# Kernel tuning notes

Hardware: AMD Instinct MI355X
Metric: run time of the kernel (lower is better)

The kernel has to match this reference:

```python
import jax, jax.numpy as jnp
import numpy as np

B, C, H, W, HEADS = 4, 32, 384, 384, 8
EPS_LN = 1e-6


def conv2d(x, w, b=None, pad=0, groups=1):
    out = jax.lax.conv_general_dilated(
        x, w, window_strides=(1, 1), padding=[(pad, pad), (pad, pad)],
        dimension_numbers=('NCHW', 'OIHW', 'NCHW'), feature_group_count=groups)
    return out if b is None else out + b[None, :, None, None]


def setup_inputs() -> dict:
    key = jax.random.key(0)
    ks = jax.random.split(key, 24)
    p = lambda k, shape: jax.random.normal(k, shape, jnp.float32) * 0.05
    return {
        'x': jax.random.normal(ks[0], (B, C, H, W), jnp.float32),
        # MCC core params (bias=False)
        'ln_w': jnp.ones((C,), jnp.float32),
        'ln_b': jnp.zeros((C,), jnp.float32),
        'temperature': jnp.ones((HEADS, 1, 1), jnp.float32),
        'pw_w': p(ks[1], (3 * C, C, 1, 1)),
        'dw_w': p(ks[2], (3 * C, 1, 3, 3)),
        'proj_w': p(ks[3], (C, C, 1, 1)),
        'ff1_w': p(ks[4], (C, C, 1, 1)),
        'ffdw_w': p(ks[5], (C, 1, 3, 3)),
        # color-space detector (convs have default bias=True)
        'det_w1': p(ks[6], (64, 32, 3, 3)), 'det_b1': jnp.zeros((64,), jnp.float32),
        'det_w2': p(ks[7], (128, 64, 3, 3)), 'det_b2': jnp.zeros((128,), jnp.float32),
        'det_w3': p(ks[8], (256, 128, 3, 3)), 'det_b3': jnp.zeros((256,), jnp.float32),
        'det_fc_w': p(ks[9], (3, 256)), 'det_fc_b': jnp.zeros((3,), jnp.float32),
        # HVI->RGB model
        'hvi_w1': p(ks[10], (64, 32, 3, 3)), 'hvi_b1': jnp.zeros((64,), jnp.float32),
        'hvi_w2': p(ks[11], (32, 64, 3, 3)), 'hvi_b2': jnp.zeros((32,), jnp.float32),
        # YCbCr->RGB model
        'ycc_w1': p(ks[12], (64, 32, 3, 3)), 'ycc_b1': jnp.zeros((64,), jnp.float32),
        'ycc_w2': p(ks[13], (32, 64, 3, 3)), 'ycc_b2': jnp.zeros((32,), jnp.float32),
    }


def _mcc_forward(x, ln_w, ln_b, temperature, pw_w, dw_w, proj_w, ff1_w, ffdw_w,
                 det_w1, det_b1, det_w2, det_b2, det_w3, det_b3, det_fc_w, det_fc_b,
                 hvi_w1, hvi_b1, hvi_w2, hvi_b2, ycc_w1, ycc_b1, ycc_w2, ycc_b2):
    relu = jax.nn.relu
    # ---- auto color-space detection ----
    f = relu(conv2d(x, det_w1, det_b1, pad=1))
    f = relu(conv2d(f, det_w2, det_b2, pad=1))
    f = relu(conv2d(f, det_w3, det_b3, pad=1))
    f = f.mean(axis=(2, 3))                      # adaptive avg pool -> [B, 256]
    logits = f @ det_fc_w.T + det_fc_b           # [B, 3]
    pred = jnp.argmax(logits[0])                 # torch uses predicted[0].item()

    def rgb_branch(xx):
        return xx

    def hvi_branch(xx):
        return relu(conv2d(relu(conv2d(xx, hvi_w1, hvi_b1, pad=1)), hvi_w2, hvi_b2, pad=1))

    def ycc_branch(xx):
        return relu(conv2d(relu(conv2d(xx, ycc_w1, ycc_b1, pad=1)), ycc_w2, ycc_b2, pad=1))

    x = jax.lax.switch(pred, [rgb_branch, hvi_branch, ycc_branch], x)

    # ---- channels_first LayerNorm ----
    u = x.mean(axis=1, keepdims=True)
    s = ((x - u) ** 2).mean(axis=1, keepdims=True)
    a = (x - u) / jnp.sqrt(s + EPS_LN)
    a = ln_w[None, :, None, None] * a + ln_b[None, :, None, None]

    # ---- qkv: 1x1 pwconv then 3x3 depthwise ----
    qkv = conv2d(conv2d(a, pw_w, pad=0), dw_w, pad=1, groups=3 * C)  # [B, 3C, H, W]
    q, k, v = jnp.split(qkv, 3, axis=1)
    ch = C // HEADS                                # channels per head
    hw = H * W
    q = q.reshape(B, HEADS, ch, hw)
    k = k.reshape(B, HEADS, ch, hw)
    v = v.reshape(B, HEADS, ch, hw)
    # L2-normalize over spatial dim (F.normalize, eps=1e-12)
    q = q / jnp.maximum(jnp.linalg.norm(q, axis=-1, keepdims=True), 1e-12)
    k = k / jnp.maximum(jnp.linalg.norm(k, axis=-1, keepdims=True), 1e-12)
    # channel-wise transposed attention: [B, heads, ch, ch]
    attn = jnp.einsum('bhcn,bhdn->bhcd', q, k) * temperature
    attn = jax.nn.softmax(attn, axis=-1)
    out = jnp.einsum('bhcd,bhdn->bhcn', attn, v).reshape(B, C, H, W)
    out = conv2d(out, proj_w, pad=0)

    # ---- feedforward on residual ----
    y = out + x
    y = jax.nn.gelu(conv2d(y, ff1_w, pad=0), approximate=False)
    y = jax.nn.gelu(conv2d(y, ffdw_w, pad=1, groups=C), approximate=False)
    return y


def reference(x, ln_w, ln_b, temperature, pw_w, dw_w, proj_w, ff1_w, ffdw_w,
              det_w1, det_b1, det_w2, det_b2, det_w3, det_b3, det_fc_w, det_fc_b,
              hvi_w1, hvi_b1, hvi_w2, hvi_b2, ycc_w1, ycc_b1, ycc_w2, ycc_b2):
    return _mcc_forward(x, ln_w, ln_b, temperature, pw_w, dw_w, proj_w, ff1_w, ffdw_w,
                        det_w1, det_b1, det_w2, det_b2, det_w3, det_b3, det_fc_w, det_fc_b,
                        hvi_w1, hvi_b1, hvi_w2, hvi_b2, ycc_w1, ycc_b1, ycc_w2, ycc_b2)
```

## Files before the change

kernel.cpp:

```cpp
#include <hip/hip_runtime.h>
#include <hip/hip_bf16.h>
#include <math.h>

#define HH 384
#define WW 384
#define HWSZ (HH*WW)
#define BB 4

typedef __attribute__((ext_vector_type(8))) short short8;
typedef __attribute__((ext_vector_type(4))) float f32x4;

static const size_t OFF_MISC = 0;
static const size_t OFF_A    = 16384;
static const size_t OFF_BW   = OFF_A + 56623104;
static const size_t MISC_POOLED = 0;
static const size_t MISC_PRED   = 1024;
static const size_t MISC_STATS  = 1056;
static const size_t MISC_MB     = 2048;

#define LPAD 40

__device__ __forceinline__ float waveSum(float v) {
#pragma unroll
    for (int off = 32; off > 0; off >>= 1) v += __shfl_down(v, off);
    return v;
}

__device__ __forceinline__ float gelu_exact(float v) {
    return 0.5f * v * (1.0f + erff(v * 0.70710678118654752f));
}

__device__ __forceinline__ unsigned short f2bf(float f) {
    __hip_bfloat16 h = __float2bfloat16(f);
    return *(unsigned short*)&h;
}
__device__ __forceinline__ float bf2f(unsigned short u) {
    unsigned int b = ((unsigned int)u) << 16;
    return __uint_as_float(b);
}

__device__ __forceinline__ void dwconv8(const float* __restrict__ base,
                                        const float* __restrict__ w9,
                                        int y, int xg, float o[8])
{
#pragma unroll
    for (int j = 0; j < 8; ++j) o[j] = 0.f;
#pragma unroll
    for (int dy = 0; dy < 3; ++dy) {
        int gy = y + dy - 1;
        if ((unsigned)gy >= (unsigned)HH) continue;
        const float* rp = base + (size_t)gy * WW + xg;
        f32x4 m0 = *(const f32x4*)(rp);
        f32x4 m1 = *(const f32x4*)(rp + 4);
        float r0 = (xg > 0) ? rp[-1] : 0.f;
        float r9 = (xg + 8 < WW) ? rp[8] : 0.f;
        float r[10] = {r0, m0[0], m0[1], m0[2], m0[3],
                           m1[0], m1[1], m1[2], m1[3], r9};
        float w0 = w9[dy * 3 + 0], w1 = w9[dy * 3 + 1], w2 = w9[dy * 3 + 2];
#pragma unroll
        for (int j = 0; j < 8; ++j)
            o[j] = fmaf(r[j], w0, fmaf(r[j + 1], w1, fmaf(r[j + 2], w2, o[j])));
    }
}


__global__ __launch_bounds__(256) void xcvt_kernel(
    const float* __restrict__ x, unsigned short* __restrict__ x0)
{
    int px = blockIdx.x * 256 + threadIdx.x;
    if (px >= HWSZ) return;
    unsigned short u[32];
#pragma unroll
    for (int c = 0; c < 32; ++c) u[c] = f2bf(x[(size_t)c * HWSZ + px]);
    uint4* dst = (uint4*)(x0 + (size_t)px * 32);
#pragma unroll
    for (int g = 0; g < 4; ++g) {
        uint4 v;
        v.x = (unsigned)u[g*8+0] | ((unsigned)u[g*8+1] << 16);
        v.y = (unsigned)u[g*8+2] | ((unsigned)u[g*8+3] << 16);
        v.z = (unsigned)u[g*8+4] | ((unsigned)u[g*8+5] << 16);
        v.w = (unsigned)u[g*8+6] | ((unsigned)u[g*8+7] << 16);
        dst[g] = v;
    }
}

__global__ __launch_bounds__(256) void wcvt_kernel(
    const float* __restrict__ w, unsigned short* __restrict__ wp,
    int Cin, int total)
{
    int t = blockIdx.x * 256 + threadIdx.x;
    if (t >= total) return;
    int nine_cin = 9 * Cin;
    int co = t / nine_cin;
    int r = t - co * nine_cin;
    int e = r / Cin;
    int ci = r - e * Cin;
    wp[t] = f2bf(w[(size_t)co * nine_cin + ci * 9 + e]);
}

template<int CIN, int COUT>
__global__ __launch_bounds__(256) void mfma_conv2_kernel(
    const unsigned short* __restrict__ in,
    const unsigned short* __restrict__ wp,
    const float* __restrict__ bias,
    unsigned short* __restrict__ out)
{
    constexpr int NT = COUT / 64;
    __shared__ unsigned short s_in[198 * LPAD];

    const int tid  = threadIdx.x;
    const int lane = tid & 63;
    const int wave = tid >> 6;
    const int nl   = lane & 15;
    const int quad = lane >> 4;
    const int row  = blockIdx.x / 6;
    const int x0   = (blockIdx.x % 6) * 64;
    const int co_w0 = wave * (COUT / 4);

    f32x4 acc[4][NT];
#pragma unroll
    for (int pg = 0; pg < 4; ++pg)
#pragma unroll
        for (int ct = 0; ct < NT; ++ct) acc[pg][ct] = (f32x4){0.f,0.f,0.f,0.f};

#pragma unroll
    for (int ci0 = 0; ci0 < CIN; ci0 += 32) {
        __syncthreads();
        for (int idx = tid; idx < 792; idx += 256) {
            int qs   = idx & 3;
            int cell = idx >> 2;
            int px   = cell % 66;
            int r    = cell / 66;
            int gy   = row + r - 1;
            int gx   = x0 + px - 1;
            uint4 v = {0u,0u,0u,0u};
            if ((unsigned)gy < (unsigned)HH && (unsigned)gx < (unsigned)WW)
                v = *(const uint4*)(in + (size_t)(gy * WW + gx) * CIN + ci0 + qs * 8);
            *(uint4*)(s_in + cell * LPAD + qs * 8) = v;
        }
        __syncthreads();
#pragma unroll
        for (int e = 0; e < 9; ++e) {
            const int er = e / 3, ec = e % 3;
            short8 bfrag[4];
#pragma unroll
            for (int pg = 0; pg < 4; ++pg)
                bfrag[pg] = *(const short8*)(s_in + ((er * 66 + pg * 16 + nl + ec) * LPAD + quad * 8));
#pragma unroll
            for (int ct = 0; ct < NT; ++ct) {
                short8 afrag = *(const short8*)(wp
                    + (size_t)(co_w0 + ct * 16 + nl) * (9 * CIN) + e * CIN + ci0 + quad * 8);
#pragma unroll
                for (int pg = 0; pg < 4; ++pg)
                    acc[pg][ct] = __builtin_amdgcn_mfma_f32_16x16x32_bf16(afrag, bfrag[pg], acc[pg][ct], 0, 0, 0);
            }
        }
    }

#pragma unroll
    for (int pg = 0; pg < 4; ++pg) {
        int px = x0 + pg * 16 + nl;
        unsigned short* op = out + ((size_t)row * WW + px) * COUT;
#pragma unroll
        for (int ct = 0; ct < NT; ++ct) {
            int cb = co_w0 + ct * 16 + quad * 4;
            ushort4 v;
            v.x = f2bf(fmaxf(acc[pg][ct][0] + bias[cb + 0], 0.f));
            v.y = f2bf(fmaxf(acc[pg][ct][1] + bias[cb + 1], 0.f));
            v.z = f2bf(fmaxf(acc[pg][ct][2] + bias[cb + 2], 0.f));
            v.w = f2bf(fmaxf(acc[pg][ct][3] + bias[cb + 3], 0.f));
            *(ushort4*)(op + cb) = v;
        }
    }
}

__global__ __launch_bounds__(256) void pool_kernel(
    const unsigned short* __restrict__ d3, float* __restrict__ pooled)
{
    __shared__ float s_pool[256];
    int t = threadIdx.x;
    s_pool[t] = 0.f;
    __syncthreads();
    int co8 = (t & 31) * 8;
    int pxg = t >> 5;
    float sums[8];
#pragma unroll
    for (int j = 0; j < 8; ++j) sums[j] = 0.f;
    int base = blockIdx.x * 2304 + pxg;
    for (int i = 0; i < 288; ++i) {
        int px = base + i * 8;
        const uint4* p = (const uint4*)(d3 + (size_t)px * 256 + co8);
        uint4 v = *p;
        unsigned int w[4] = {v.x, v.y, v.z, v.w};
#pragma unroll
        for (int g = 0; g < 4; ++g) {
            sums[g*2+0] += bf2f((unsigned short)(w[g] & 0xFFFF));
            sums[g*2+1] += bf2f((unsigned short)(w[g] >> 16));
        }
    }
#pragma unroll
    for (int j = 0; j < 8; ++j) atomicAdd(&s_pool[co8 + j], sums[j]);
    __syncthreads();
    atomicAdd(&pooled[t], s_pool[t]);
}

__global__ void fc_argmax_kernel(const float* __restrict__ pooled,
                                 const float* __restrict__ fcw,
                                 const float* __restrict__ fcb,
                                 int* __restrict__ pred)
{
    int t = threadIdx.x;
    float m = pooled[t] * (1.0f / (float)HWSZ);
    float p0 = m * fcw[t];
    float p1 = m * fcw[256 + t];
    float p2 = m * fcw[512 + t];
    p0 = waveSum(p0); p1 = waveSum(p1); p2 = waveSum(p2);
    __shared__ float rr[3][4];
    int wid = t >> 6, lane = t & 63;
    if (lane == 0) { rr[0][wid] = p0; rr[1][wid] = p1; rr[2][wid] = p2; }
    __syncthreads();
    if (t == 0) {
        float l0 = rr[0][0] + rr[0][1] + rr[0][2] + rr[0][3] + fcb[0];
        float l1 = rr[1][0] + rr[1][1] + rr[1][2] + rr[1][3] + fcb[1];
        float l2 = rr[2][0] + rr[2][1] + rr[2][2] + rr[2][3] + fcb[2];
        int best = 0; float bv = l0;
        if (l1 > bv) { best = 1; bv = l1; }
        if (l2 > bv) { best = 2; bv = l2; }
        *pred = best;
    }
}


__global__ __launch_bounds__(256) void wsplit_kernel(
    const float* __restrict__ w,
    unsigned short* __restrict__ hi, unsigned short* __restrict__ lo,
    int Cin, int total)
{
    int t = blockIdx.x * 256 + threadIdx.x;
    if (t >= total) return;
    int nine_cin = 9 * Cin;
    int co = t / nine_cin;
    int r = t - co * nine_cin;
    int e = r / Cin;
    int ci = r - e * Cin;
    float v = w[(size_t)co * nine_cin + ci * 9 + e];
    unsigned short h = f2bf(v);
    hi[t] = h;
    lo[t] = f2bf(v - bf2f(h));
}

__global__ __launch_bounds__(256) void xsplitb_kernel(
    const float* __restrict__ x, const int* __restrict__ predp,
    unsigned short* __restrict__ hi, unsigned short* __restrict__ lo)
{
    if (__builtin_amdgcn_readfirstlane(*predp) == 0) return;
    int p = blockIdx.x * 256 + threadIdx.x;
    if (p >= BB * HWSZ) return;
    int b = p / HWSZ, n = p % HWSZ;
    const float* sp = x + (size_t)b * 32 * HWSZ + n;
    unsigned short uh[32], ul[32];
#pragma unroll
    for (int c = 0; c < 32; ++c) {
        float v = sp[(size_t)c * HWSZ];
        unsigned short h = f2bf(v);
        uh[c] = h;
        ul[c] = f2bf(v - bf2f(h));
    }
    uint4* dh = (uint4*)(hi + (size_t)p * 32);
    uint4* dl = (uint4*)(lo + (size_t)p * 32);
#pragma unroll
    for (int g = 0; g < 4; ++g) {
        uint4 vh, vl;
        vh.x = (unsigned)uh[g*8+0] | ((unsigned)uh[g*8+1] << 16);
        vh.y = (unsigned)uh[g*8+2] | ((unsigned)uh[g*8+3] << 16);
        vh.z = (unsigned)uh[g*8+4] | ((unsigned)uh[g*8+5] << 16);
        vh.w = (unsigned)uh[g*8+6] | ((unsigned)uh[g*8+7] << 16);
        vl.x = (unsigned)ul[g*8+0] | ((unsigned)ul[g*8+1] << 16);
        vl.y = (unsigned)ul[g*8+2] | ((unsigned)ul[g*8+3] << 16);
        vl.z = (unsigned)ul[g*8+4] | ((unsigned)ul[g*8+5] << 16);
        vl.w = (unsigned)ul[g*8+6] | ((unsigned)ul[g*8+7] << 16);
        dh[g] = vh;
        dl[g] = vl;
    }
}

template<int CIN, int COUT, int OUTMODE>
__global__ __launch_bounds__(256) void bconv_kernel(
    const unsigned short* __restrict__ in_hi, const unsigned short* __restrict__ in_lo,
    const unsigned short* __restrict__ wAh, const unsigned short* __restrict__ wAl,
    const unsigned short* __restrict__ wBh, const unsigned short* __restrict__ wBl,
    const float* __restrict__ bA, const float* __restrict__ bB,
    const int* __restrict__ predp,
    unsigned short* __restrict__ out_hi, unsigned short* __restrict__ out_lo,
    float* __restrict__ out_f32)
{
    const int p = __builtin_amdgcn_readfirstlane(*predp);
    if (p == 0) return;
    const unsigned short* whi = (p == 1) ? wAh : wBh;
    const unsigned short* wlo = (p == 1) ? wAl : wBl;
    const float* bias = (p == 1) ? bA : bB;

    constexpr int NPG = (COUT == 64) ? 4 : 2;
    __shared__ unsigned short s_hi[198 * LPAD];
    __shared__ unsigned short s_lo[198 * LPAD];

    const int tid  = threadIdx.x;
    const int lane = tid & 63;
    const int wave = tid >> 6;
    const int nl   = lane & 15;
    const int quad = lane >> 4;
    const int row  = blockIdx.x / 6;
    const int x0   = (blockIdx.x % 6) * 64;
    const int b    = blockIdx.y;
    const int co_w0 = (COUT == 64) ? wave * 16 : (wave & 1) * 16;
    const int pg0   = (COUT == 64) ? 0 : (wave >> 1) * 2;

    f32x4 acc[NPG];
#pragma unroll
    for (int g = 0; g < NPG; ++g) acc[g] = (f32x4){0.f,0.f,0.f,0.f};

    const unsigned short* ibh = in_hi + (size_t)b * HWSZ * CIN;
    const unsigned short* ibl = in_lo + (size_t)b * HWSZ * CIN;

#pragma unroll
    for (int ci0 = 0; ci0 < CIN; ci0 += 32) {
        __syncthreads();
        for (int idx = tid; idx < 792; idx += 256) {
            int qs   = idx & 3;
            int cell = idx >> 2;
            int px   = cell % 66;
            int r    = cell / 66;
            int gy   = row + r - 1;
            int gx   = x0 + px - 1;
            uint4 vh = {0u,0u,0u,0u}, vl = {0u,0u,0u,0u};
            if ((unsigned)gy < (unsigned)HH && (unsigned)gx < (unsigned)WW) {
                size_t base = (size_t)(gy * WW + gx) * CIN + ci0 + qs * 8;
                vh = *(const uint4*)(ibh + base);
                vl = *(const uint4*)(ibl + base);
            }
            *(uint4*)(s_hi + cell * LPAD + qs * 8) = vh;
            *(uint4*)(s_lo + cell * LPAD + qs * 8) = vl;
        }
        __syncthreads();
#pragma unroll
        for (int e = 0; e < 9; ++e) {
            const int er = e / 3, ec = e % 3;
            size_t woff = (size_t)(co_w0 + nl) * (9 * CIN) + e * CIN + ci0 + quad * 8;
            short8 ah = *(const short8*)(whi + woff);
            short8 al = *(const short8*)(wlo + woff);
#pragma unroll
            for (int g = 0; g < NPG; ++g) {
                int cell = er * 66 + (pg0 + g) * 16 + nl + ec;
                short8 bh = *(const short8*)(s_hi + cell * LPAD + quad * 8);
                short8 bl = *(const short8*)(s_lo + cell * LPAD + quad * 8);
                acc[g] = __builtin_amdgcn_mfma_f32_16x16x32_bf16(ah, bh, acc[g], 0, 0, 0);
                acc[g] = __builtin_amdgcn_mfma_f32_16x16x32_bf16(ah, bl, acc[g], 0, 0, 0);
                acc[g] = __builtin_amdgcn_mfma_f32_16x16x32_bf16(al, bh, acc[g], 0, 0, 0);
            }
        }
    }

    const int cb = co_w0 + quad * 4;
#pragma unroll
    for (int g = 0; g < NPG; ++g) {
        int px = x0 + (pg0 + g) * 16 + nl;
        float r0 = fmaxf(acc[g][0] + bias[cb + 0], 0.f);
        float r1 = fmaxf(acc[g][1] + bias[cb + 1], 0.f);
        float r2 = fmaxf(acc[g][2] + bias[cb + 2], 0.f);
        float r3 = fmaxf(acc[g][3] + bias[cb + 3], 0.f);
        if (OUTMODE == 0) {
            size_t base = ((size_t)b * HWSZ + row * WW + px) * COUT + cb;
            ushort4 vh, vl;
            unsigned short h;
            h = f2bf(r0); vh.x = h; vl.x = f2bf(r0 - bf2f(h));
            h = f2bf(r1); vh.y = h; vl.y = f2bf(r1 - bf2f(h));
            h = f2bf(r2); vh.z = h; vl.z = f2bf(r2 - bf2f(h));
            h = f2bf(r3); vh.w = h; vl.w = f2bf(r3 - bf2f(h));
            *(ushort4*)(out_hi + base) = vh;
            *(ushort4*)(out_lo + base) = vl;
        } else {
            size_t sp = (size_t)row * WW + px;
            out_f32[((size_t)b * COUT + cb + 0) * HWSZ + sp] = r0;
            out_f32[((size_t)b * COUT + cb + 1) * HWSZ + sp] = r1;
            out_f32[((size_t)b * COUT + cb + 2) * HWSZ + sp] = r2;
            out_f32[((size_t)b * COUT + cb + 3) * HWSZ + sp] = r3;
        }
    }
}

__global__ __launch_bounds__(256) void lnpw_kernel(
    const float* __restrict__ x, const float* __restrict__ xb,
    const int* __restrict__ predp,
    const float* __restrict__ lnw, const float* __restrict__ lnb,
    const float* __restrict__ pww,
    float* __restrict__ qkvp)
{
    int p = blockIdx.x * 256 + threadIdx.x;
    if (p >= BB * HWSZ) return;
    int pr = __builtin_amdgcn_readfirstlane(*predp);
    const float* src = (pr == 0) ? x : xb;
    int b = p / HWSZ, n = p % HWSZ;
    const float* sp = src + (size_t)b * 32 * HWSZ + n;
    float v[32];
    float mean = 0.f;
#pragma unroll
    for (int c = 0; c < 32; ++c) { v[c] = sp[(size_t)c * HWSZ]; mean += v[c]; }
    mean *= (1.f / 32.f);
    float var = 0.f;
#pragma unroll
    for (int c = 0; c < 32; ++c) { float d = v[c] - mean; var += d * d; }
    var *= (1.f / 32.f);
    float rstd = rsqrtf(var + 1e-6f);
#pragma unroll
    for (int c = 0; c < 32; ++c)
        v[c] = (v[c] - mean) * rstd * lnw[c] + lnb[c];

    float acc[96];
#pragma unroll
    for (int co = 0; co < 96; ++co) acc[co] = 0.f;
    for (int ci = 0; ci < 32; ++ci) {
        float va = v[ci];
#pragma unroll
        for (int co = 0; co < 96; ++co)
            acc[co] = fmaf(pww[co * 32 + ci], va, acc[co]);
    }
    float* op = qkvp + (size_t)b * 96 * HWSZ + n;
#pragma unroll
    for (int co = 0; co < 96; ++co) op[(size_t)co * HWSZ] = acc[co];
}

__global__ __launch_bounds__(256) void qkdwstats_kernel(
    const float* __restrict__ qkvp, const float* __restrict__ dww,
    float* __restrict__ stats)
{
    __shared__ float s_t[4][6][392];
    __shared__ float red[4][24];

    const int bh = blockIdx.y;
    const int b = bh >> 3, h = bh & 7;
    const float* qbase = qkvp + ((size_t)b * 96 + h * 4) * HWSZ;
    const float* kbase = qkvp + ((size_t)b * 96 + 32 + h * 4) * HWSZ;
    const float* wq = dww + (h * 4) * 9;
    const float* wk = dww + (32 + h * 4) * 9;

    const int tid  = threadIdx.x;
    const int w    = tid >> 6;
    const int lane = tid & 63;
    const int y0   = blockIdx.x * 4;

    if (tid < 48) {
        int ch = tid / 12, rem = tid % 12;
        int r = rem >> 1, side = rem & 1;
        s_t[ch][r][side ? 388 : 3] = 0.f;
    }

    float s[16], qn[4], kn[4];
#pragma unroll
    for (int i = 0; i < 16; ++i) s[i] = 0.f;
#pragma unroll
    for (int i = 0; i < 4; ++i) { qn[i] = 0.f; kn[i] = 0.f; }

    {
#pragma unroll
        for (int i = 0; i < 9; ++i) {
            int idx = i * 256 + tid;
            int ch  = idx / 576;
            int rem = idx - ch * 576;
            int r   = rem / 96;
            int g   = rem - r * 96;
            int gy  = y0 + r - 1;
            f32x4 v = {0.f, 0.f, 0.f, 0.f};
            if ((unsigned)gy < (unsigned)HH)
                v = *(const f32x4*)(qbase + (size_t)ch * HWSZ + (size_t)gy * WW + g * 4);
            *(f32x4*)&s_t[ch][r][g * 4 + 4] = v;
        }
    }
    __syncthreads();

    float q[4][6];
#pragma unroll
    for (int ch = 0; ch < 4; ++ch) {
        const float* w9 = wq + ch * 9;
#pragma unroll
        for (int jj = 0; jj < 6; ++jj) {
            int colL = jj * 64 + lane + 4;
            float acc = 0.f;
#pragma unroll
            for (int dy = 0; dy < 3; ++dy) {
                const float* rr = &s_t[ch][w + dy][0];
                acc = fmaf(rr[colL - 1], w9[dy * 3 + 0], acc);
                acc = fmaf(rr[colL    ], w9[dy * 3 + 1], acc);
                acc = fmaf(rr[colL + 1], w9[dy * 3 + 2], acc);
            }
            q[ch][jj] = acc;
            qn[ch] = fmaf(acc, acc, qn[ch]);
        }
    }
    __syncthreads();

    {
#pragma unroll
        for (int i = 0; i < 9; ++i) {
            int idx = i * 256 + tid;
            int ch  = idx / 576;
            int rem = idx - ch * 576;
            int r   = rem / 96;
            int g   = rem - r * 96;
            int gy  = y0 + r - 1;
            f32x4 v = {0.f, 0.f, 0.f, 0.f};
            if ((unsigned)gy < (unsigned)HH)
                v = *(const f32x4*)(kbase + (size_t)ch * HWSZ + (size_t)gy * WW + g * 4);
            *(f32x4*)&s_t[ch][r][g * 4 + 4] = v;
        }
    }
    __syncthreads();

#pragma unroll
    for (int d = 0; d < 4; ++d) {
        const float* w9 = wk + d * 9;
#pragma unroll
        for (int jj = 0; jj < 6; ++jj) {
            int colL = jj * 64 + lane + 4;
            float kv = 0.f;
#pragma unroll
            for (int dy = 0; dy < 3; ++dy) {
                const float* rr = &s_t[d][w + dy][0];
                kv = fmaf(rr[colL - 1], w9[dy * 3 + 0], kv);
                kv = fmaf(rr[colL    ], w9[dy * 3 + 1], kv);
                kv = fmaf(rr[colL + 1], w9[dy * 3 + 2], kv);
            }
            kn[d] = fmaf(kv, kv, kn[d]);
#pragma unroll
            for (int c = 0; c < 4; ++c)
                s[c * 4 + d] = fmaf(q[c][jj], kv, s[c * 4 + d]);
        }
    }

#pragma unroll
    for (int i = 0; i < 16; ++i) {
        float v = waveSum(s[i]);
        if (lane == 0) red[w][i] = v;
    }
#pragma unroll
    for (int i = 0; i < 4; ++i) {
        float v = waveSum(qn[i]);
        if (lane == 0) red[w][16 + i] = v;
        float u = waveSum(kn[i]);
        if (lane == 0) red[w][20 + i] = u;
    }
    __syncthreads();
    if (tid < 24) {
        float v = red[0][tid] + red[1][tid] + red[2][tid] + red[3][tid];
        atomicAdd(&stats[bh * 24 + tid], v);
    }
}

__global__ __launch_bounds__(256) void vdw_kernel(
    float* __restrict__ qkvp, const float* __restrict__ dww)
{
    int t = blockIdx.x * 256 + threadIdx.x;
    int bc = t / 18432;
    int g  = t - bc * 18432;
    int b = bc >> 5, c = bc & 31;
    int y  = g / 48;
    int xg = (g - y * 48) * 8;
    const float* ip = qkvp + ((size_t)b * 96 + 64 + c) * HWSZ;
    const float* wc = dww + (64 + c) * 9;
    float o[8];
    dwconv8(ip, wc, y, xg, o);
    float* op = qkvp + ((size_t)b * 96 + c) * HWSZ + (size_t)y * WW + xg;
    f32x4 v0 = {o[0], o[1], o[2], o[3]};
    f32x4 v1 = {o[4], o[5], o[6], o[7]};
    *(f32x4*)op = v0;
    *(f32x4*)(op + 4) = v1;
}

__global__ void attnmb_kernel(const float* __restrict__ stats,
                              const float* __restrict__ temp,
                              const float* __restrict__ projw,
                              float* __restrict__ Mb)
{
    __shared__ float attn_s[4][8][4][4];
    int t = threadIdx.x;
    if (t < 128) {
        int b = t >> 5;
        int h = (t >> 2) & 7;
        int c = t & 3;
        const float* st = stats + (b * 8 + h) * 24;
        float qn = fmaxf(sqrtf(st[16 + c]), 1e-12f);
        float tp = temp[h];
        float raw[4];
#pragma unroll
        for (int d = 0; d < 4; ++d) {
            float kn = fmaxf(sqrtf(st[20 + d]), 1e-12f);
            raw[d] = st[c * 4 + d] / (qn * kn) * tp;
        }
        float m = fmaxf(fmaxf(raw[0], raw[1]), fmaxf(raw[2], raw[3]));
        float e0 = expf(raw[0] - m), e1 = expf(raw[1] - m);
        float e2 = expf(raw[2] - m), e3 = expf(raw[3] - m);
        float inv = 1.f / (e0 + e1 + e2 + e3);
        attn_s[b][h][c][0] = e0 * inv;
        attn_s[b][h][c][1] = e1 * inv;
        attn_s[b][h][c][2] = e2 * inv;
        attn_s[b][h][c][3] = e3 * inv;
    }
    __syncthreads();
    for (int idx = t; idx < 4096; idx += 256) {
        int b = idx >> 10;
        int r = idx & 1023;
        int co = r >> 5;
        int j = r & 31;
        int h = j >> 2;
        int d = j & 3;
        float m = 0.f;
#pragma unroll
        for (int l = 0; l < 4; ++l)
            m = fmaf(projw[co * 32 + h * 4 + l], attn_s[b][h][l][d], m);
        Mb[idx] = m;
    }
}

__global__ __launch_bounds__(256) void e1_kernel(
    float* __restrict__ qkvp, const float* __restrict__ x,
    const float* __restrict__ xb, const int* __restrict__ predp,
    const float* __restrict__ Mb, const float* __restrict__ ff1w)
{
    int p = blockIdx.x * 256 + threadIdx.x;
    if (p >= BB * HWSZ) return;
    int pr = __builtin_amdgcn_readfirstlane(*predp);
    const float* src = (pr == 0) ? x : xb;
    int b = p / HWSZ, n = p % HWSZ;
    float* vp = qkvp + (size_t)b * 96 * HWSZ + n;
    const float* Mbb = Mb + b * 1024;
    float y[32];
#pragma unroll
    for (int c = 0; c < 32; ++c) y[c] = 0.f;
    for (int j = 0; j < 32; ++j) {
        float vj = vp[(size_t)j * HWSZ];
#pragma unroll
        for (int co = 0; co < 32; ++co)
            y[co] = fmaf(Mbb[co * 32 + j], vj, y[co]);
    }
    const float* xp = src + (size_t)b * 32 * HWSZ + n;
#pragma unroll
    for (int c = 0; c < 32; ++c) y[c] += xp[(size_t)c * HWSZ];
    for (int co = 0; co < 32; ++co) {
        float s = 0.f;
#pragma unroll
        for (int ci = 0; ci < 32; ++ci)
            s = fmaf(ff1w[co * 32 + ci], y[ci], s);
        vp[(size_t)co * HWSZ] = gelu_exact(s);
    }
}

__global__ __launch_bounds__(256) void fdw_kernel(
    const float* __restrict__ z1, const float* __restrict__ w,
    float* __restrict__ out)
{
    int t = blockIdx.x * 256 + threadIdx.x;
    int bc = t / 18432;
    int g  = t - bc * 18432;
    int b = bc >> 5, c = bc & 31;
    int y  = g / 48;
    int xg = (g - y * 48) * 8;
    const float* ip = z1 + ((size_t)b * 96 + c) * HWSZ;
    const float* wc = w + c * 9;
    float o[8];
    dwconv8(ip, wc, y, xg, o);
#pragma unroll
    for (int j = 0; j < 8; ++j) o[j] = gelu_exact(o[j]);
    float* op = out + ((size_t)b * 32 + c) * HWSZ + (size_t)y * WW + xg;
    f32x4 v0 = {o[0], o[1], o[2], o[3]};
    f32x4 v1 = {o[4], o[5], o[6], o[7]};
    *(f32x4*)op = v0;
    *(f32x4*)(op + 4) = v1;
}

extern "C" void kernel_launch(void* const* d_in, const int* in_sizes, int n_in,
                              void* d_out, int out_size, void* d_ws, size_t ws_size,
                              hipStream_t stream)
{
    (void)in_sizes; (void)n_in; (void)out_size; (void)ws_size;
    const float* x      = (const float*)d_in[0];
    const float* ln_w   = (const float*)d_in[1];
    const float* ln_b   = (const float*)d_in[2];
    const float* temp   = (const float*)d_in[3];
    const float* pw_w   = (const float*)d_in[4];
    const float* dw_w   = (const float*)d_in[5];
    const float* proj_w = (const float*)d_in[6];
    const float* ff1_w  = (const float*)d_in[7];
    const float* ffdw_w = (const float*)d_in[8];
    const float* det_w1 = (const float*)d_in[9];
    const float* det_b1 = (const float*)d_in[10];
    const float* det_w2 = (const float*)d_in[11];
    const float* det_b2 = (const float*)d_in[12];
    const float* det_w3 = (const float*)d_in[13];
    const float* det_b3 = (const float*)d_in[14];
    const float* fc_w   = (const float*)d_in[15];
    const float* fc_b   = (const float*)d_in[16];
    const float* hvi_w1 = (const float*)d_in[17];
    const float* hvi_b1 = (const float*)d_in[18];
    const float* hvi_w2 = (const float*)d_in[19];
    const float* hvi_b2 = (const float*)d_in[20];
    const float* ycc_w1 = (const float*)d_in[21];
    const float* ycc_b1 = (const float*)d_in[22];
    const float* ycc_w2 = (const float*)d_in[23];
    const float* ycc_b2 = (const float*)d_in[24];

    float* ws     = (float*)d_ws;
    float* misc   = ws + OFF_MISC;
    float* A      = ws + OFF_A;
    unsigned short* x0bf  = (unsigned short*)A;
    unsigned short* f1bf  = (unsigned short*)(A + 2359296);
    unsigned short* f2bf  = (unsigned short*)(A + 7077888);
    unsigned short* d3out = (unsigned short*)(A + 16515072);
    unsigned short* w1p   = (unsigned short*)(A + 56423104);
    unsigned short* w2p   = (unsigned short*)(A + 56432320);
    unsigned short* w3p   = (unsigned short*)(A + 56469184);
    unsigned short* xs_hi = (unsigned short*)A;
    unsigned short* xs_lo = (unsigned short*)(A + 9437184);
    unsigned short* t1_hi = (unsigned short*)(A + 18874368);
    unsigned short* t1_lo = (unsigned short*)(A + 37748736);
    unsigned short* bw    = (unsigned short*)(ws + OFF_BW);
    unsigned short* bw_h1h = bw;            unsigned short* bw_h1l = bw + 18432;
    unsigned short* bw_y1h = bw + 36864;    unsigned short* bw_y1l = bw + 55296;
    unsigned short* bw_h2h = bw + 73728;    unsigned short* bw_h2l = bw + 92160;
    unsigned short* bw_y2h = bw + 110592;   unsigned short* bw_y2l = bw + 129024;
    float* qkvp   = A;
    float* xb     = (float*)d_out;
    float* pooled = misc + MISC_POOLED;
    int*   pred   = (int*)(misc + MISC_PRED);
    float* stats  = misc + MISC_STATS;
    float* Mb     = misc + MISC_MB;
    float* out    = (float*)d_out;

    hipMemsetAsync(misc, 0, 2048 * sizeof(float), stream);

    dim3 blk(256);
    wcvt_kernel<<<(18432 + 255) / 256, blk, 0, stream>>>(det_w1, w1p, 32, 18432);
    wcvt_kernel<<<(73728 + 255) / 256, blk, 0, stream>>>(det_w2, w2p, 64, 73728);
    wcvt_kernel<<<(294912 + 255) / 256, blk, 0, stream>>>(det_w3, w3p, 128, 294912);
    xcvt_kernel<<<576, blk, 0, stream>>>(x, x0bf);
    wsplit_kernel<<<72, blk, 0, stream>>>(hvi_w1, bw_h1h, bw_h1l, 32, 18432);
    wsplit_kernel<<<72, blk, 0, stream>>>(ycc_w1, bw_y1h, bw_y1l, 32, 18432);
    wsplit_kernel<<<72, blk, 0, stream>>>(hvi_w2, bw_h2h, bw_h2l, 64, 18432);
    wsplit_kernel<<<72, blk, 0, stream>>>(ycc_w2, bw_y2h, bw_y2l, 64, 18432);

    mfma_conv2_kernel<32, 64>  <<<2304, blk, 0, stream>>>(x0bf, w1p, det_b1, f1bf);
    mfma_conv2_kernel<64, 128> <<<2304, blk, 0, stream>>>(f1bf, w2p, det_b2, f2bf);
    mfma_conv2_kernel<128, 256><<<2304, blk, 0, stream>>>(f2bf, w3p, det_b3, d3out);
    pool_kernel<<<64, blk, 0, stream>>>(d3out, pooled);
    fc_argmax_kernel<<<1, 256, 0, stream>>>(pooled, fc_w, fc_b, pred);

    xsplitb_kernel<<<2304, blk, 0, stream>>>(x, pred, xs_hi, xs_lo);
    bconv_kernel<32, 64, 0><<<dim3(2304, BB), blk, 0, stream>>>(
        xs_hi, xs_lo, bw_h1h, bw_h1l, bw_y1h, bw_y1l, hvi_b1, ycc_b1, pred,
        t1_hi, t1_lo, nullptr);
    bconv_kernel<64, 32, 1><<<dim3(2304, BB), blk, 0, stream>>>(
        t1_hi, t1_lo, bw_h2h, bw_h2l, bw_y2h, bw_y2l, hvi_b2, ycc_b2, pred,
        nullptr, nullptr, xb);

    lnpw_kernel<<<2304, blk, 0, stream>>>(x, xb, pred, ln_w, ln_b, pw_w, qkvp);

    qkdwstats_kernel<<<dim3(96, 32), blk, 0, stream>>>(qkvp, dw_w, stats);
    vdw_kernel<<<9216, blk, 0, stream>>>(qkvp, dw_w);
    attnmb_kernel<<<1, 256, 0, stream>>>(stats, temp, proj_w, Mb);

    e1_kernel<<<2304, blk, 0, stream>>>(qkvp, x, xb, pred, Mb, ff1_w);
    fdw_kernel<<<9216, blk, 0, stream>>>(qkvp, ffdw_w, out);
}
```

Before: 1.239 ms.

## Tile bconv over four output rows per block to reuse the input halo

The split-bf16 3x3 conv kernel now computes four output rows per block, one per wave, and each wave covers all output channels, instead of one row per block. The shared-memory halo tile grows to six rows, so input loads are amortized over four rows rather than three-row reloads per row, and weight fragments are reused across four pixel groups. The grid shrinks to a quarter of the blocks. This raises accumulator register pressure (up to 16 f32x4 accumulators for COUT=64) and LDS use, which may lower occupancy.

```diff
diff --git a/kernel.cpp b/kernel.cpp
--- a/kernel.cpp
+++ b/kernel.cpp
@@ -300,24 +300,24 @@
     const unsigned short* wlo = (p == 1) ? wAl : wBl;
     const float* bias = (p == 1) ? bA : bB;
 
-    constexpr int NPG = (COUT == 64) ? 4 : 2;
-    __shared__ unsigned short s_hi[198 * LPAD];
-    __shared__ unsigned short s_lo[198 * LPAD];
+    constexpr int NCT = COUT / 16;
+    __shared__ unsigned short s_hi[396 * LPAD];
+    __shared__ unsigned short s_lo[396 * LPAD];
 
     const int tid  = threadIdx.x;
     const int lane = tid & 63;
     const int wave = tid >> 6;
     const int nl   = lane & 15;
     const int quad = lane >> 4;
-    const int row  = blockIdx.x / 6;
+    const int y0   = (blockIdx.x / 6) * 4;
     const int x0   = (blockIdx.x % 6) * 64;
     const int b    = blockIdx.y;
-    const int co_w0 = (COUT == 64) ? wave * 16 : (wave & 1) * 16;
-    const int pg0   = (COUT == 64) ? 0 : (wave >> 1) * 2;
-
-    f32x4 acc[NPG];
-#pragma unroll
-    for (int g = 0; g < NPG; ++g) acc[g] = (f32x4){0.f,0.f,0.f,0.f};
+
+    f32x4 acc[4][NCT];
+#pragma unroll
+    for (int pg = 0; pg < 4; ++pg)
+#pragma unroll
+        for (int ct = 0; ct < NCT; ++ct) acc[pg][ct] = (f32x4){0.f,0.f,0.f,0.f};
 
     const unsigned short* ibh = in_hi + (size_t)b * HWSZ * CIN;
     const unsigned short* ibl = in_lo + (size_t)b * HWSZ * CIN;
@@ -325,12 +325,12 @@
 #pragma unroll
     for (int ci0 = 0; ci0 < CIN; ci0 += 32) {
         __syncthreads();
-        for (int idx = tid; idx < 792; idx += 256) {
+        for (int idx = tid; idx < 1584; idx += 256) {
             int qs   = idx & 3;
             int cell = idx >> 2;
             int px   = cell % 66;
             int r    = cell / 66;
-            int gy   = row + r - 1;
+            int gy   = y0 + r - 1;
             int gx   = x0 + px - 1;
             uint4 vh = {0u,0u,0u,0u}, vl = {0u,0u,0u,0u};
             if ((unsigned)gy < (unsigned)HH && (unsigned)gx < (unsigned)WW) {
@@ -345,45 +345,56 @@
 #pragma unroll
         for (int e = 0; e < 9; ++e) {
             const int er = e / 3, ec = e % 3;
-            size_t woff = (size_t)(co_w0 + nl) * (9 * CIN) + e * CIN + ci0 + quad * 8;
-            short8 ah = *(const short8*)(whi + woff);
-            short8 al = *(const short8*)(wlo + woff);
-#pragma unroll
-            for (int g = 0; g < NPG; ++g) {
-                int cell = er * 66 + (pg0 + g) * 16 + nl + ec;
-                short8 bh = *(const short8*)(s_hi + cell * LPAD + quad * 8);
-                short8 bl = *(const short8*)(s_lo + cell * LPAD + quad * 8);
-                acc[g] = __builtin_amdgcn_mfma_f32_16x16x32_bf16(ah, bh, acc[g], 0, 0, 0);
-                acc[g] = __builtin_amdgcn_mfma_f32_16x16x32_bf16(ah, bl, acc[g], 0, 0, 0);
-                acc[g] = __builtin_amdgcn_mfma_f32_16x16x32_bf16(al, bh, acc[g], 0, 0, 0);
+            short8 bh[4], bl[4];
+#pragma unroll
+            for (int pg = 0; pg < 4; ++pg) {
+                int cell = (wave + er) * 66 + pg * 16 + nl + ec;
+                bh[pg] = *(const short8*)(s_hi + cell * LPAD + quad * 8);
+                bl[pg] = *(const short8*)(s_lo + cell * LPAD + quad * 8);
             }
-        }
-    }
-
-    const int cb = co_w0 + quad * 4;
-#pragma unroll
-    for (int g = 0; g < NPG; ++g) {
-        int px = x0 + (pg0 + g) * 16 + nl;
-        float r0 = fmaxf(acc[g][0] + bias[cb + 0], 0.f);
-        float r1 = fmaxf(acc[g][1] + bias[cb + 1], 0.f);
-        float r2 = fmaxf(acc[g][2] + bias[cb + 2], 0.f);
-        float r3 = fmaxf(acc[g][3] + bias[cb + 3], 0.f);
-        if (OUTMODE == 0) {
-            size_t base = ((size_t)b * HWSZ + row * WW + px) * COUT + cb;
-            ushort4 vh, vl;
-            unsigned short h;
-            h = f2bf(r0); vh.x = h; vl.x = f2bf(r0 - bf2f(h));
-            h = f2bf(r1); vh.y = h; vl.y = f2bf(r1 - bf2f(h));
-            h = f2bf(r2); vh.z = h; vl.z = f2bf(r2 - bf2f(h));
-            h = f2bf(r3); vh.w = h; vl.w = f2bf(r3 - bf2f(h));
-            *(ushort4*)(out_hi + base) = vh;
-            *(ushort4*)(out_lo + base) = vl;
-        } else {
-            size_t sp = (size_t)row * WW + px;
-            out_f32[((size_t)b * COUT + cb + 0) * HWSZ + sp] = r0;
-            out_f32[((size_t)b * COUT + cb + 1) * HWSZ + sp] = r1;
-            out_f32[((size_t)b * COUT + cb + 2) * HWSZ + sp] = r2;
-            out_f32[((size_t)b * COUT + cb + 3) * HWSZ + sp] = r3;
+#pragma unroll
+            for (int ct = 0; ct < NCT; ++ct) {
+                size_t woff = (size_t)(ct * 16 + nl) * (9 * CIN) + e * CIN + ci0 + quad * 8;
+                short8 ah = *(const short8*)(whi + woff);
+                short8 al = *(const short8*)(wlo + woff);
+#pragma unroll
+                for (int pg = 0; pg < 4; ++pg) {
+                    acc[pg][ct] = __builtin_amdgcn_mfma_f32_16x16x32_bf16(ah, bh[pg], acc[pg][ct], 0, 0, 0);
+                    acc[pg][ct] = __builtin_amdgcn_mfma_f32_16x16x32_bf16(ah, bl[pg], acc[pg][ct], 0, 0, 0);
+                    acc[pg][ct] = __builtin_amdgcn_mfma_f32_16x16x32_bf16(al, bh[pg], acc[pg][ct], 0, 0, 0);
+                }
+            }
+        }
+    }
+
+    const int row = y0 + wave;
+#pragma unroll
+    for (int pg = 0; pg < 4; ++pg) {
+        int px = x0 + pg * 16 + nl;
+#pragma unroll
+        for (int ct = 0; ct < NCT; ++ct) {
+            int cb = ct * 16 + quad * 4;
+            float r0 = fmaxf(acc[pg][ct][0] + bias[cb + 0], 0.f);
+            float r1 = fmaxf(acc[pg][ct][1] + bias[cb + 1], 0.f);
+            float r2 = fmaxf(acc[pg][ct][2] + bias[cb + 2], 0.f);
+            float r3 = fmaxf(acc[pg][ct][3] + bias[cb + 3], 0.f);
+            if (OUTMODE == 0) {
+                size_t base = ((size_t)b * HWSZ + row * WW + px) * COUT + cb;
+                ushort4 vh, vl;
+                unsigned short h;
+                h = f2bf(r0); vh.x = h; vl.x = f2bf(r0 - bf2f(h));
+                h = f2bf(r1); vh.y = h; vl.y = f2bf(r1 - bf2f(h));
+                h = f2bf(r2); vh.z = h; vl.z = f2bf(r2 - bf2f(h));
+                h = f2bf(r3); vh.w = h; vl.w = f2bf(r3 - bf2f(h));
+                *(ushort4*)(out_hi + base) = vh;
+                *(ushort4*)(out_lo + base) = vl;
+            } else {
+                size_t sp = (size_t)row * WW + px;
+                out_f32[((size_t)b * COUT + cb + 0) * HWSZ + sp] = r0;
+                out_f32[((size_t)b * COUT + cb + 1) * HWSZ + sp] = r1;
+                out_f32[((size_t)b * COUT + cb + 2) * HWSZ + sp] = r2;
+                out_f32[((size_t)b * COUT + cb + 3) * HWSZ + sp] = r3;
+            }
         }
     }
 }
@@ -753,10 +764,10 @@
     fc_argmax_kernel<<<1, 256, 0, stream>>>(pooled, fc_w, fc_b, pred);
 
     xsplitb_kernel<<<2304, blk, 0, stream>>>(x, pred, xs_hi, xs_lo);
-    bconv_kernel<32, 64, 0><<<dim3(2304, BB), blk, 0, stream>>>(
+    bconv_kernel<32, 64, 0><<<dim3(576, BB), blk, 0, stream>>>(
         xs_hi, xs_lo, bw_h1h, bw_h1l, bw_y1h, bw_y1l, hvi_b1, ycc_b1, pred,
         t1_hi, t1_lo, nullptr);
-    bconv_kernel<64, 32, 1><<<dim3(2304, BB), blk, 0, stream>>>(
+    bconv_kernel<64, 32, 1><<<dim3(576, BB), blk, 0, stream>>>(
         t1_hi, t1_lo, bw_h2h, bw_h2l, bw_y2h, bw_y2l, hvi_b2, ycc_b2, pred,
         nullptr, nullptr, xb);
 
```

Result: no change. 1.226 ms (-1.0%).
